# Optimization experiments

Hardware: AMD Instinct MI355X
Metric: run time of the kernel (lower is better)

## Reference

```python
import jax, jax.numpy as jnp
import numpy as np

B, A, C, M = 4, 120000, 80, 32
ALPHA, GAMMA, EPS = 0.75, 2.0, 1e-4
STD = np.array([0.1, 0.1, 0.2, 0.2, 0.1, 0.1, 0.2, 0.2], dtype=np.float32)


def _make_boxes(key, shape, img=1024.0):
    k1, k2, k3, k4 = jax.random.split(key, 4)
    cx = jax.random.uniform(k1, shape) * img
    cy = jax.random.uniform(k2, shape) * img
    w = jax.random.uniform(k3, shape) * 224.0 + 32.0
    h = jax.random.uniform(k4, shape) * 224.0 + 32.0
    return jnp.stack([cx - 0.5 * w, cy - 0.5 * h, cx + 0.5 * w, cy + 0.5 * h], axis=-1)


def setup_inputs() -> dict:
    key = jax.random.key(0)
    kc, kr, ka, kh, kf, kl, ki = jax.random.split(key, 7)
    classifications = jax.random.uniform(kc, (B, A, C), dtype=jnp.float32)
    regressions = jax.random.normal(kr, (B, A, 8), dtype=jnp.float32)
    anchors = _make_boxes(ka, (1, A))  # [1,A,4]
    head = _make_boxes(kh, (B, M))     # [B,M,4]
    full = _make_boxes(kf, (B, M))     # [B,M,4]
    labels = jax.random.randint(kl, (B, M, 1), 0, C).astype(jnp.float32)
    ignore = jax.random.randint(ki, (B, M, 1), 0, 2).astype(jnp.float32)
    annotations = jnp.concatenate([head, full, labels, ignore], axis=-1)  # [B,M,10]
    return {"classifications": classifications, "regressions": regressions,
            "anchors": anchors, "annotations": annotations}


def _calc_iou(a, b):
    # a: [A,4], b: [B,M,4] -> [B,A,M]
    area_b = (b[..., 2] - b[..., 0]) * (b[..., 3] - b[..., 1])  # [B,M]
    a = a[None, :, None, :]
    bb = b[:, None, :, :]
    iw = jnp.clip(jnp.minimum(a[..., 2], bb[..., 2]) - jnp.maximum(a[..., 0], bb[..., 0]), 0.0)
    ih = jnp.clip(jnp.minimum(a[..., 3], bb[..., 3]) - jnp.maximum(a[..., 1], bb[..., 1]), 0.0)
    area_a = ((a[..., 2] - a[..., 0]) * (a[..., 3] - a[..., 1]))  # [1,A,1]
    inter = iw * ih
    ua = jnp.clip(area_a + area_b[:, None, :] - inter, 1e-8)
    return inter / ua


def reference(classifications, regressions, anchors, annotations):
    anchor = anchors[0]                       # [A,4]
    aw = anchor[:, 2] - anchor[:, 0]
    ah = anchor[:, 3] - anchor[:, 1]
    acx = anchor[:, 0] + 0.5 * aw
    acy = anchor[:, 1] + 0.5 * ah

    ann = annotations[..., :-1]               # [B,M,9]
    full_box = ann[..., 4:8]

    iou = _calc_iou(anchor, full_box)         # [B,A,M]
    iou_max = jnp.max(iou, axis=-1)           # [B,A]
    iou_arg = jnp.argmax(iou, axis=-1)        # [B,A]

    pos = iou_max >= 0.5                      # [B,A]
    neg = iou_max < 0.4
    num_pos = jnp.sum(pos, axis=1).astype(jnp.float32)  # [B]

    assigned = jnp.take_along_axis(ann, iou_arg[..., None], axis=1)  # [B,A,9]
    assigned_cls = assigned[..., 8].astype(jnp.int32)                # [B,A]

    one_hot = jax.nn.one_hot(assigned_cls, classifications.shape[-1], dtype=jnp.float32)
    targets = jnp.where(pos[..., None], one_hot,
                        jnp.where(neg[..., None], 0.0, -1.0))        # [B,A,C]

    p = jnp.clip(classifications, EPS, 1.0 - EPS)
    alpha_f = jnp.where(targets == 1.0, ALPHA, 1.0 - ALPHA)
    focal_w = alpha_f * jnp.where(targets == 1.0, 1.0 - p, p) ** GAMMA
    bce = -(targets * jnp.log(p) + (1.0 - targets) * jnp.log(1.0 - p))
    cls_loss = jnp.where(targets != -1.0, focal_w * bce, 0.0)
    cls_losses = jnp.sum(cls_loss, axis=(1, 2)) / jnp.clip(num_pos, 1.0)  # [B]

    gw_h = assigned[..., 2] - assigned[..., 0]
    gh_h = assigned[..., 3] - assigned[..., 1]
    gcx_h = assigned[..., 0] + 0.5 * gw_h
    gcy_h = assigned[..., 1] + 0.5 * gh_h
    gw_f = assigned[..., 6] - assigned[..., 4]
    gh_f = assigned[..., 7] - assigned[..., 5]
    gcx_f = assigned[..., 4] + 0.5 * gw_f
    gcy_f = assigned[..., 5] + 0.5 * gh_f
    gw_h = jnp.clip(gw_h, 1.0); gh_h = jnp.clip(gh_h, 1.0)
    gw_f = jnp.clip(gw_f, 1.0); gh_f = jnp.clip(gh_f, 1.0)

    t = jnp.stack([
        (gcx_f - acx) / aw, (gcy_f - acy) / ah,
        jnp.log(gw_f / aw), jnp.log(gh_f / ah),
        (gcx_h - acx) / aw * 4.0, (gcy_h - acy) / ah * 4.0,
        jnp.log(gw_h / aw * 4.0), jnp.log(gh_h / ah * 4.0),
    ], axis=-1) / jnp.asarray(STD)            # [B,A,8]

    diff = jnp.abs(t - regressions)
    # only_full=True: weights zero out cols 4:8
    diff = diff * jnp.asarray([1., 1., 1., 1., 0., 0., 0., 0.], dtype=jnp.float32)
    rl = jnp.where(diff <= 1.0 / 9.0, 0.5 * 9.0 * diff * diff, diff - 0.5 / 9.0)
    rl4 = rl[..., 0:4] * pos[..., None]       # [B,A,4], only positive anchors
    reg_losses = jnp.where(num_pos > 0,
                           jnp.sum(rl4, axis=(1, 2)) / (jnp.clip(num_pos, 1.0) * 4.0),
                           0.0)               # mean over positive rows x 4 cols

    return (jnp.mean(cls_losses, keepdims=True), jnp.mean(reg_losses, keepdims=True))
```

## Files before the change

kernel.cpp:

```cpp
#include <hip/hip_runtime.h>

#define NB 4
#define NA 120000
#define NC 80
#define NM 32

#define ALPHA_ 0.75f
#define EPS_   1e-4f

constexpr int BLOCK = 256;
constexpr int APB   = 256;
constexpr int F4_PER_ANCHOR = NC / 4;

__device__ __forceinline__ float wave_reduce(float v) {
    #pragma unroll
    for (int off = 32; off > 0; off >>= 1) v += __shfl_down(v, off, 64);
    return v;
}

__device__ __forceinline__ float focal_term(float x, int meta, int c) {
    float p = fminf(fmaxf(x, EPS_), 1.0f - EPS_);
    if (meta == c) {
        float q = 1.0f - p;
        return ALPHA_ * q * q * (-logf(p));
    } else {
        return (1.0f - ALPHA_) * p * p * (-logf(1.0f - p));
    }
}

__global__ __launch_bounds__(BLOCK)
void focal_main(const float* __restrict__ cls,
                const float* __restrict__ reg,
                const float* __restrict__ anchors,
                const float* __restrict__ ann,
                double* __restrict__ acc)
{
    __shared__ float s_ann[NM * 10];
    __shared__ int   s_meta[APB];
    __shared__ float s_red[3][4];

    const int b   = blockIdx.y;
    const int a0  = blockIdx.x * APB;
    const int tid = threadIdx.x;

    for (int i = tid; i < NM * 10; i += BLOCK)
        s_ann[i] = ann[b * NM * 10 + i];
    __syncthreads();

    float regLoss = 0.0f;
    float posCnt  = 0.0f;
    const int a = a0 + tid;

    if (a < NA) {
        const float4 an = ((const float4*)anchors)[a];
        const float ax1 = an.x, ay1 = an.y, ax2 = an.z, ay2 = an.w;
        const float aw  = ax2 - ax1, ah = ay2 - ay1;
        const float acx = ax1 + 0.5f * aw, acy = ay1 + 0.5f * ah;
        const float areaA = aw * ah;

        float best = -1.0f;
        int   arg  = 0;
        #pragma unroll
        for (int m = 0; m < NM; ++m) {
            const float bx1 = s_ann[m * 10 + 4];
            const float by1 = s_ann[m * 10 + 5];
            const float bx2 = s_ann[m * 10 + 6];
            const float by2 = s_ann[m * 10 + 7];
            float iw = fminf(ax2, bx2) - fmaxf(ax1, bx1); iw = fmaxf(iw, 0.0f);
            float ih = fminf(ay2, by2) - fmaxf(ay1, by1); ih = fmaxf(ih, 0.0f);
            const float inter = iw * ih;
            const float areaB = (bx2 - bx1) * (by2 - by1);
            const float ua    = fmaxf(areaA + areaB - inter, 1e-8f);
            const float iou   = inter / ua;
            if (iou > best) { best = iou; arg = m; }
        }

        int meta;
        if (best >= 0.5f) {
            meta   = (int)s_ann[arg * 10 + 8];
            posCnt = 1.0f;
            const float fx1 = s_ann[arg * 10 + 4];
            const float fy1 = s_ann[arg * 10 + 5];
            const float fx2 = s_ann[arg * 10 + 6];
            const float fy2 = s_ann[arg * 10 + 7];
            float gw = fx2 - fx1, gh = fy2 - fy1;
            const float gcx = fx1 + 0.5f * gw, gcy = fy1 + 0.5f * gh;
            gw = fmaxf(gw, 1.0f); gh = fmaxf(gh, 1.0f);
            const float t0 = ((gcx - acx) / aw) / 0.1f;
            const float t1 = ((gcy - acy) / ah) / 0.1f;
            const float t2 = logf(gw / aw) / 0.2f;
            const float t3 = logf(gh / ah) / 0.2f;
            const float4 r4 = ((const float4*)reg)[(size_t)(b * NA + a) * 2];
            const float d0 = fabsf(t0 - r4.x);
            const float d1 = fabsf(t1 - r4.y);
            const float d2 = fabsf(t2 - r4.z);
            const float d3 = fabsf(t3 - r4.w);
            const float beta = 1.0f / 9.0f;
            #define SL1(d) ((d) <= beta ? 4.5f * (d) * (d) : (d) - 0.5f / 9.0f)
            regLoss = SL1(d0) + SL1(d1) + SL1(d2) + SL1(d3);
            #undef SL1
        } else if (best < 0.4f) {
            meta = -1;
        } else {
            meta = -2;
        }
        s_meta[tid] = meta;
    } else {
        s_meta[tid] = -2;
    }
    __syncthreads();

    float clsSum = 0.0f;
    const float4* cls4 = (const float4*)(cls + (size_t)b * NA * NC);
    #pragma unroll
    for (int it = 0; it < APB * F4_PER_ANCHOR / BLOCK; ++it) {
        const int idx = it * BLOCK + tid;
        const int la  = idx / F4_PER_ANCHOR;
        const int c4  = idx % F4_PER_ANCHOR;
        const int ga  = a0 + la;
        const int meta = s_meta[la];
        if (meta != -2 && ga < NA) {
            const float4 p4 = cls4[(size_t)ga * F4_PER_ANCHOR + c4];
            const int cb = c4 * 4;
            clsSum += focal_term(p4.x, meta, cb + 0);
            clsSum += focal_term(p4.y, meta, cb + 1);
            clsSum += focal_term(p4.z, meta, cb + 2);
            clsSum += focal_term(p4.w, meta, cb + 3);
        }
    }

    const int wave = tid >> 6, lane = tid & 63;
    float rc = wave_reduce(clsSum);
    float rr = wave_reduce(regLoss);
    float rp = wave_reduce(posCnt);
    if (lane == 0) { s_red[0][wave] = rc; s_red[1][wave] = rr; s_red[2][wave] = rp; }
    __syncthreads();
    if (tid == 0) {
        float c = s_red[0][0] + s_red[0][1] + s_red[0][2] + s_red[0][3];
        float r = s_red[1][0] + s_red[1][1] + s_red[1][2] + s_red[1][3];
        float p = s_red[2][0] + s_red[2][1] + s_red[2][2] + s_red[2][3];
        atomicAdd(&acc[b * 3 + 0], (double)c);
        atomicAdd(&acc[b * 3 + 1], (double)r);
        atomicAdd(&acc[b * 3 + 2], (double)p);
    }
}

__global__ void focal_finalize(const double* __restrict__ acc, float* __restrict__ out) {
    double clsTot = 0.0, regTot = 0.0;
    #pragma unroll
    for (int b = 0; b < NB; ++b) {
        const double np  = acc[b * 3 + 2];
        const double npc = np < 1.0 ? 1.0 : np;
        clsTot += acc[b * 3 + 0] / npc;
        regTot += (np > 0.0) ? acc[b * 3 + 1] / (npc * 4.0) : 0.0;
    }
    out[0] = (float)(clsTot / NB);
    out[1] = (float)(regTot / NB);
}

extern "C" void kernel_launch(void* const* d_in, const int* in_sizes, int n_in,
                              void* d_out, int out_size, void* d_ws, size_t ws_size,
                              hipStream_t stream) {
    const float* cls     = (const float*)d_in[0];
    const float* reg     = (const float*)d_in[1];
    const float* anchors = (const float*)d_in[2];
    const float* ann     = (const float*)d_in[3];
    float* out = (float*)d_out;
    double* acc = (double*)d_ws;

    hipMemsetAsync(acc, 0, NB * 3 * sizeof(double), stream);

    dim3 grid((NA + APB - 1) / APB, NB);
    focal_main<<<grid, BLOCK, 0, stream>>>(cls, reg, anchors, ann, acc);
    focal_finalize<<<1, 1, 0, stream>>>(acc, out);
}
```

Before: 271.7 us.

## Rewrite focal loss as uniform negative term plus per-anchor positive correction

The class loop now computes the negative-class focal term for every element, scaled by a per-anchor coefficient stored in shared memory (zero for ignored anchors). For positive anchors it adds a single correction that swaps the negative term for the positive one at the labelled class. This removes the per-element label compare and branch. Logs use the hardware log2 builtin, divisions become multiplies, and the block is resized to 192 so 120000 divides exactly, which drops the bounds checks. Ignored anchors' class rows are now always loaded rather than skipped, and the fast log2 may differ slightly in precision.

```diff
diff --git a/kernel.cpp b/kernel.cpp
--- a/kernel.cpp
+++ b/kernel.cpp
@@ -7,10 +7,12 @@
 
 #define ALPHA_ 0.75f
 #define EPS_   1e-4f
+#define LN2_   0.69314718055994531f
 
-constexpr int BLOCK = 256;
-constexpr int APB   = 256;
+constexpr int BLOCK = 192;
+constexpr int APB   = 192;
 constexpr int F4_PER_ANCHOR = NC / 4;
+constexpr int P2_ITERS = APB * F4_PER_ANCHOR / BLOCK;
 
 __device__ __forceinline__ float wave_reduce(float v) {
     #pragma unroll
@@ -18,15 +20,7 @@
     return v;
 }
 
-__device__ __forceinline__ float focal_term(float x, int meta, int c) {
-    float p = fminf(fmaxf(x, EPS_), 1.0f - EPS_);
-    if (meta == c) {
-        float q = 1.0f - p;
-        return ALPHA_ * q * q * (-logf(p));
-    } else {
-        return (1.0f - ALPHA_) * p * p * (-logf(1.0f - p));
-    }
-}
+__device__ __forceinline__ float flog2(float x) { return __builtin_amdgcn_logf(x); }
 
 __global__ __launch_bounds__(BLOCK)
 void focal_main(const float* __restrict__ cls,
@@ -36,8 +30,8 @@
                 double* __restrict__ acc)
 {
     __shared__ float s_ann[NM * 10];
-    __shared__ int   s_meta[APB];
-    __shared__ float s_red[3][4];
+    __shared__ float s_coef[APB];
+    __shared__ float s_red[3][3];
 
     const int b   = blockIdx.y;
     const int a0  = blockIdx.x * APB;
@@ -49,9 +43,10 @@
 
     float regLoss = 0.0f;
     float posCnt  = 0.0f;
+    float clsCorr = 0.0f;
     const int a = a0 + tid;
 
-    if (a < NA) {
+    {
         const float4 an = ((const float4*)anchors)[a];
         const float ax1 = an.x, ay1 = an.y, ax2 = an.z, ay2 = an.w;
         const float aw  = ax2 - ax1, ah = ay2 - ay1;
@@ -75,10 +70,20 @@
             if (iou > best) { best = iou; arg = m; }
         }
 
-        int meta;
-        if (best >= 0.5f) {
-            meta   = (int)s_ann[arg * 10 + 8];
+        const bool pos = best >= 0.5f;
+        const bool neg = best < 0.4f;
+        s_coef[tid] = (pos || neg) ? (-0.25f * LN2_) : 0.0f;
+
+        if (pos) {
             posCnt = 1.0f;
+            const int c = (int)s_ann[arg * 10 + 8];
+            const float x  = cls[((size_t)b * NA + a) * NC + c];
+            const float p  = fminf(fmaxf(x, EPS_), 1.0f - EPS_);
+            const float q  = 1.0f - p;
+            const float posT = 0.75f * q * q * (-LN2_ * flog2(p));
+            const float negT = 0.25f * p * p * (-LN2_ * flog2(q));
+            clsCorr = posT - negT;
+
             const float fx1 = s_ann[arg * 10 + 4];
             const float fy1 = s_ann[arg * 10 + 5];
             const float fx2 = s_ann[arg * 10 + 6];
@@ -86,10 +91,10 @@
             float gw = fx2 - fx1, gh = fy2 - fy1;
             const float gcx = fx1 + 0.5f * gw, gcy = fy1 + 0.5f * gh;
             gw = fmaxf(gw, 1.0f); gh = fmaxf(gh, 1.0f);
-            const float t0 = ((gcx - acx) / aw) / 0.1f;
-            const float t1 = ((gcy - acy) / ah) / 0.1f;
-            const float t2 = logf(gw / aw) / 0.2f;
-            const float t3 = logf(gh / ah) / 0.2f;
+            const float t0 = ((gcx - acx) / aw) * 10.0f;
+            const float t1 = ((gcy - acy) / ah) * 10.0f;
+            const float t2 = (LN2_ * flog2(gw / aw)) * 5.0f;
+            const float t3 = (LN2_ * flog2(gh / ah)) * 5.0f;
             const float4 r4 = ((const float4*)reg)[(size_t)(b * NA + a) * 2];
             const float d0 = fabsf(t0 - r4.x);
             const float d1 = fabsf(t1 - r4.y);
@@ -99,34 +104,30 @@
             #define SL1(d) ((d) <= beta ? 4.5f * (d) * (d) : (d) - 0.5f / 9.0f)
             regLoss = SL1(d0) + SL1(d1) + SL1(d2) + SL1(d3);
             #undef SL1
-        } else if (best < 0.4f) {
-            meta = -1;
-        } else {
-            meta = -2;
         }
-        s_meta[tid] = meta;
-    } else {
-        s_meta[tid] = -2;
     }
     __syncthreads();
 
-    float clsSum = 0.0f;
-    const float4* cls4 = (const float4*)(cls + (size_t)b * NA * NC);
+    float clsSum = clsCorr;
+    const float4* cls4 = (const float4*)(cls + (size_t)b * NA * NC) + (size_t)a0 * F4_PER_ANCHOR;
     #pragma unroll
-    for (int it = 0; it < APB * F4_PER_ANCHOR / BLOCK; ++it) {
+    for (int it = 0; it < P2_ITERS; ++it) {
         const int idx = it * BLOCK + tid;
         const int la  = idx / F4_PER_ANCHOR;
-        const int c4  = idx % F4_PER_ANCHOR;
-        const int ga  = a0 + la;
-        const int meta = s_meta[la];
-        if (meta != -2 && ga < NA) {
-            const float4 p4 = cls4[(size_t)ga * F4_PER_ANCHOR + c4];
-            const int cb = c4 * 4;
-            clsSum += focal_term(p4.x, meta, cb + 0);
-            clsSum += focal_term(p4.y, meta, cb + 1);
-            clsSum += focal_term(p4.z, meta, cb + 2);
-            clsSum += focal_term(p4.w, meta, cb + 3);
-        }
+        const float C = s_coef[la];
+        const float4 x4 = cls4[idx];
+
+        float p0 = fminf(fmaxf(x4.x, EPS_), 1.0f - EPS_);
+        float p1 = fminf(fmaxf(x4.y, EPS_), 1.0f - EPS_);
+        float p2 = fminf(fmaxf(x4.z, EPS_), 1.0f - EPS_);
+        float p3 = fminf(fmaxf(x4.w, EPS_), 1.0f - EPS_);
+
+        float t0 = p0 * p0 * flog2(1.0f - p0);
+        float t1 = p1 * p1 * flog2(1.0f - p1);
+        float t2 = p2 * p2 * flog2(1.0f - p2);
+        float t3 = p3 * p3 * flog2(1.0f - p3);
+
+        clsSum = fmaf((t0 + t1) + (t2 + t3), C, clsSum);
     }
 
     const int wave = tid >> 6, lane = tid & 63;
@@ -136,9 +137,9 @@
     if (lane == 0) { s_red[0][wave] = rc; s_red[1][wave] = rr; s_red[2][wave] = rp; }
     __syncthreads();
     if (tid == 0) {
-        float c = s_red[0][0] + s_red[0][1] + s_red[0][2] + s_red[0][3];
-        float r = s_red[1][0] + s_red[1][1] + s_red[1][2] + s_red[1][3];
-        float p = s_red[2][0] + s_red[2][1] + s_red[2][2] + s_red[2][3];
+        float c = s_red[0][0] + s_red[0][1] + s_red[0][2];
+        float r = s_red[1][0] + s_red[1][1] + s_red[1][2];
+        float p = s_red[2][0] + s_red[2][1] + s_red[2][2];
         atomicAdd(&acc[b * 3 + 0], (double)c);
         atomicAdd(&acc[b * 3 + 1], (double)r);
         atomicAdd(&acc[b * 3 + 2], (double)p);
@@ -170,7 +171,7 @@
 
     hipMemsetAsync(acc, 0, NB * 3 * sizeof(double), stream);
 
-    dim3 grid((NA + APB - 1) / APB, NB);
+    dim3 grid(NA / APB, NB);
     focal_main<<<grid, BLOCK, 0, stream>>>(cls, reg, anchors, ann, acc);
     focal_finalize<<<1, 1, 0, stream>>>(acc, out);
 }
```

Result: faster. 264.2 us (-2.8%).
